# Performance work log

Hardware: AMD Instinct MI355X
Metric: run time of the kernel (lower is better)

Reference implementation:

```python
import jax, jax.numpy as jnp
import numpy as np

# CustomConvLayer with a 3x3-tap .kof file, global defaults:
#   operation: x * w, input_encode: x, kernel_encode: w
# => out[b,o,h,w] = sum_c sum_k x_pad[b,c,h+dh_k,w+dw_k] * weights[o,c,k]
# Tap offsets: integer stencil (dh,dw) in {0,1,2}^2 (k_elems=9), padding=1, stride=1.

PAD = 1
TAPS = [(dh, dw) for dh in range(3) for dw in range(3)]  # 9 taps


def setup_inputs() -> dict:
    key = jax.random.key(0)
    k1, k2 = jax.random.split(key)
    x = jax.random.normal(k1, (16, 64, 128, 128), dtype=jnp.float32)
    # learned per-tap weights: [out_channels, in_channels, k_elems]
    weights = jax.random.normal(k2, (128, 64, 9), dtype=jnp.float32) * 0.05
    return {"x": x, "weights": weights}


def reference(x, weights):
    B, C, H, Wd = x.shape
    xp = jnp.pad(x, ((0, 0), (0, 0), (PAD, PAD), (PAD, PAD)))
    # gather per-tap shifted views: [B, C, K, H, W]
    gathered = jnp.stack([xp[:, :, dh:dh + H, dw:dw + Wd] for dh, dw in TAPS], axis=2)
    # per-tap op x*w, then combine over in_channels and taps
    out = jnp.einsum('bckhw,ock->bohw', gathered, weights)
    return out
```

## Files before the change

### kernel.cpp

```cpp
#include <hip/hip_runtime.h>
#include <hip/hip_bf16.h>
#include <stdint.h>


typedef __bf16 bf16x8 __attribute__((ext_vector_type(8)));
typedef float  f32x4  __attribute__((ext_vector_type(4)));

#define GLD_TO_LDS16(g, l)                                                        \
  __builtin_amdgcn_global_load_lds((const __attribute__((address_space(1))) void*)(g), \
                                   (__attribute__((address_space(3))) void*)(l), 16, 0, 0)

__global__ __launch_bounds__(256) void xform_x(const float* __restrict__ x,
                                               __bf16* __restrict__ xpad) {
  __shared__ float tile[64][129];
  const int tid = threadIdx.x;
  const int b = blockIdx.x >> 7;
  const int h = blockIdx.x & 127;

  const bf16x8 z8 = {};
  __bf16* prow = xpad + (size_t)(b * 130 + h + 1) * 8320;
  if (tid < 8)        *(bf16x8*)(prow + tid * 8) = z8;
  else if (tid < 16)  *(bf16x8*)(prow + 8256 + (tid - 8) * 8) = z8;
  if (h == 0) {
    bf16x8* r0 = (bf16x8*)(xpad + (size_t)(b * 130) * 8320);
    for (int i = tid; i < 1040; i += 256) r0[i] = z8;
  } else if (h == 127) {
    bf16x8* r129 = (bf16x8*)(xpad + (size_t)(b * 130 + 129) * 8320);
    for (int i = tid; i < 1040; i += 256) r129[i] = z8;
  }

  const float* src = x + (((size_t)b * 64) * 128 + h) * 128;
  for (int i = tid; i < 2048; i += 256) {
    const int c = i >> 5, w4 = i & 31;
    f32x4 v = *(const f32x4*)(src + (size_t)c * 16384 + w4 * 4);
    tile[c][w4 * 4 + 0] = v[0];
    tile[c][w4 * 4 + 1] = v[1];
    tile[c][w4 * 4 + 2] = v[2];
    tile[c][w4 * 4 + 3] = v[3];
  }
  __syncthreads();
  __bf16* dst = xpad + ((size_t)(b * 130 + h + 1) * 130 + 1) * 64;
  for (int i = tid; i < 1024; i += 256) {
    const int w = i >> 3, cg = i & 7;
    bf16x8 o;
#pragma unroll
    for (int r = 0; r < 8; ++r) o[r] = (__bf16)tile[cg * 8 + r][w];
    *(bf16x8*)(dst + (size_t)w * 64 + cg * 8) = o;
  }
}

__global__ __launch_bounds__(256) void xform_w(const float* __restrict__ wgt,
                                               __bf16* __restrict__ BtF) {
  const int t = blockIdx.x * 256 + threadIdx.x;
  if (t >= 9216) return;
  const int s = t >> 9, rem = t & 511, quad = rem >> 7, n = rem & 127;
  bf16x8 o;
#pragma unroll
  for (int r = 0; r < 8; ++r) {
    const int k = s * 32 + quad * 8 + r;
    const int tap = k >> 6, c = k & 63;
    o[r] = (__bf16)wgt[(n * 64 + c) * 9 + tap];
  }
  *(bf16x8*)(BtF + (size_t)t * 8) = o;
}

__global__ __launch_bounds__(512, 4) void conv_mfma(const __bf16* __restrict__ xpad,
                                                    const __bf16* __restrict__ BtF,
                                                    float* __restrict__ out) {
  __shared__ alignas(16) __bf16 Aslab[4160 * 8];
  const int tid  = threadIdx.x;
  const int lane = tid & 63;
  const int wave = tid >> 6;
  const int quad = lane >> 4;
  const int l16  = lane & 15;
  const int rank = (blockIdx.x & 7) * 128 + (blockIdx.x >> 3);
  const int b  = rank >> 6;
  const int h0 = (rank & 63) << 1;
  const int wn = wave & 1;
  const int wm = wave >> 1;
  const int r  = wm >> 1;
  const int wq = (wm & 1) << 6;

  const __bf16* slab = xpad + (size_t)(b * 130 + h0) * 8320;
#define STAGE_BLK(BLK) do {                                               \
    const int l_   = ((BLK) << 6) + lane;                                 \
    const int v_   = l_ >> 3;                                             \
    const int cqs_ = (l_ & 7) ^ (v_ & 7);                                 \
    GLD_TO_LDS16(slab + v_ * 64 + cqs_ * 8, (char*)Aslab + ((BLK) << 10)); \
  } while (0)

#pragma unroll
  for (int k = 0; k < 4; ++k) STAGE_BLK(wave + (k << 3));
  STAGE_BLK(32);
  __builtin_amdgcn_sched_barrier(0);
  STAGE_BLK(33 + wave * 2);
  STAGE_BLK(34 + wave * 2);
  __builtin_amdgcn_sched_barrier(0);
  STAGE_BLK(49 + wave * 2);
  STAGE_BLK(50 + wave * 2);
  __builtin_amdgcn_sched_barrier(0);

  f32x4 acc[4][4] = {};

#define PHASE(DH)                                                              \
  _Pragma("unroll")                                                            \
  for (int dw = 0; dw < 3; ++dw) {                                             \
    _Pragma("unroll")                                                          \
    for (int half = 0; half < 2; ++half) {                                     \
      const int s_  = ((DH) * 3 + dw) * 2 + half;                              \
      const int cq_ = (half << 2) + quad;                                      \
      bf16x8 aF[4], bF[4];          \
      _Pragma("unroll")                                                        \
      for (int i = 0; i < 4; ++i) {                                            \
        const int v_    = ((DH) + r) * 130 + wq + (i << 4) + l16 + dw;         \
        const int slot_ = (v_ << 3) + (cq_ ^ (v_ & 7));                        \
        aF[i] = *(const bf16x8*)(Aslab + (size_t)slot_ * 8);                   \
        bF[i] = *(const bf16x8*)(BtF +                                         \
                 ((size_t)((s_ * 4 + quad) * 128 + (wn << 6) + (i << 4) + l16) << 3)); \
      }                                                                        \
      _Pragma("unroll")                                                        \
      for (int i = 0; i < 4; ++i)                                              \
        _Pragma("unroll")                                                      \
        for (int j = 0; j < 4; ++j)                                            \
          acc[i][j] = __builtin_amdgcn_mfma_f32_16x16x32_bf16(aF[i], bF[j],    \
                                                              acc[i][j], 0, 0, 0); \
    }                                                                          \
  }

  asm volatile("s_waitcnt vmcnt(4)" ::: "memory");
  __builtin_amdgcn_s_barrier();
  PHASE(0)
  asm volatile("s_waitcnt vmcnt(2)" ::: "memory");
  __builtin_amdgcn_s_barrier();
  PHASE(1)
  asm volatile("s_waitcnt vmcnt(0)" ::: "memory");
  __builtin_amdgcn_s_barrier();
  PHASE(2)

#pragma unroll
  for (int j = 0; j < 4; ++j) {
    const int n = (wn << 6) + (j << 4) + l16;
    float* orow = out + (((size_t)(b * 128 + n) * 128 + (h0 + r)) << 7);
#pragma unroll
    for (int i = 0; i < 4; ++i) {
      const int m0 = wq + (i << 4) + (quad << 2);
      *(f32x4*)(orow + m0) = acc[i][j];
    }
  }
}

__global__ void conv_naive(const float* __restrict__ x, const float* __restrict__ wgt,
                           float* __restrict__ out, int total) {
  int idx = blockIdx.x * 256 + threadIdx.x;
  if (idx >= total) return;
  const int w = idx & 127;
  const int h = (idx >> 7) & 127;
  const int o = (idx >> 14) & 127;
  const int b = idx >> 21;
  float s = 0.f;
  for (int c = 0; c < 64; ++c) {
    const float* xc = x + ((size_t)(b * 64 + c) * 128) * 128;
    const float* wc = wgt + (o * 64 + c) * 9;
    for (int dh = 0; dh < 3; ++dh) {
      const int hh = h + dh - 1;
      if (hh < 0 || hh >= 128) continue;
      for (int dw = 0; dw < 3; ++dw) {
        const int ww = w + dw - 1;
        if (ww < 0 || ww >= 128) continue;
        s += xc[hh * 128 + ww] * wc[dh * 3 + dw];
      }
    }
  }
  out[idx] = s;
}

extern "C" void kernel_launch(void* const* d_in, const int* in_sizes, int n_in,
                              void* d_out, int out_size, void* d_ws, size_t ws_size,
                              hipStream_t stream) {
  const float* x   = (const float*)d_in[0];
  const float* wgt = (const float*)d_in[1];
  float* out = (float*)d_out;

  const size_t BTF_BYTES  = 9216ull * 16;
  const size_t XPAD_BYTES = 16ull * 130 * 130 * 64 * sizeof(__bf16);

  if (ws_size < BTF_BYTES + XPAD_BYTES) {
    const int total = 16 * 128 * 128 * 128;
    conv_naive<<<(total + 255) / 256, 256, 0, stream>>>(x, wgt, out, total);
    return;
  }

  __bf16* BtF  = (__bf16*)d_ws;
  __bf16* xpad = (__bf16*)((char*)d_ws + BTF_BYTES);

  xform_w<<<36, 256, 0, stream>>>(wgt, BtF);
  xform_x<<<16 * 128, 256, 0, stream>>>(x, xpad);
  conv_mfma<<<1024, 512, 0, stream>>>(xpad, BtF, out);
}
```

Before: 221.0 us.

## Fuse input transpose/bf16 conversion into conv kernel, drop padded workspace

Removes the separate xform_x pass that wrote a padded NHWC bf16 copy of x, and instead has each conv block load three fp32 input rows directly, convert to bf16, and transpose through a double-buffered LDS tile into the swizzled A slab. Blocks now cover one output row with 256 threads instead of two rows with 512, and outputs use nontemporal stores. This removes the extra global round-trip and a kernel launch. In exchange each input row is read and converted by three blocks, and the staging loop has a barrier per step.

```diff
diff --git a/kernel.cpp b/kernel.cpp
--- a/kernel.cpp
+++ b/kernel.cpp
@@ -5,49 +5,6 @@
 
 typedef __bf16 bf16x8 __attribute__((ext_vector_type(8)));
 typedef float  f32x4  __attribute__((ext_vector_type(4)));
-
-#define GLD_TO_LDS16(g, l)                                                        \
-  __builtin_amdgcn_global_load_lds((const __attribute__((address_space(1))) void*)(g), \
-                                   (__attribute__((address_space(3))) void*)(l), 16, 0, 0)
-
-__global__ __launch_bounds__(256) void xform_x(const float* __restrict__ x,
-                                               __bf16* __restrict__ xpad) {
-  __shared__ float tile[64][129];
-  const int tid = threadIdx.x;
-  const int b = blockIdx.x >> 7;
-  const int h = blockIdx.x & 127;
-
-  const bf16x8 z8 = {};
-  __bf16* prow = xpad + (size_t)(b * 130 + h + 1) * 8320;
-  if (tid < 8)        *(bf16x8*)(prow + tid * 8) = z8;
-  else if (tid < 16)  *(bf16x8*)(prow + 8256 + (tid - 8) * 8) = z8;
-  if (h == 0) {
-    bf16x8* r0 = (bf16x8*)(xpad + (size_t)(b * 130) * 8320);
-    for (int i = tid; i < 1040; i += 256) r0[i] = z8;
-  } else if (h == 127) {
-    bf16x8* r129 = (bf16x8*)(xpad + (size_t)(b * 130 + 129) * 8320);
-    for (int i = tid; i < 1040; i += 256) r129[i] = z8;
-  }
-
-  const float* src = x + (((size_t)b * 64) * 128 + h) * 128;
-  for (int i = tid; i < 2048; i += 256) {
-    const int c = i >> 5, w4 = i & 31;
-    f32x4 v = *(const f32x4*)(src + (size_t)c * 16384 + w4 * 4);
-    tile[c][w4 * 4 + 0] = v[0];
-    tile[c][w4 * 4 + 1] = v[1];
-    tile[c][w4 * 4 + 2] = v[2];
-    tile[c][w4 * 4 + 3] = v[3];
-  }
-  __syncthreads();
-  __bf16* dst = xpad + ((size_t)(b * 130 + h + 1) * 130 + 1) * 64;
-  for (int i = tid; i < 1024; i += 256) {
-    const int w = i >> 3, cg = i & 7;
-    bf16x8 o;
-#pragma unroll
-    for (int r = 0; r < 8; ++r) o[r] = (__bf16)tile[cg * 8 + r][w];
-    *(bf16x8*)(dst + (size_t)w * 64 + cg * 8) = o;
-  }
-}
 
 __global__ __launch_bounds__(256) void xform_w(const float* __restrict__ wgt,
                                                __bf16* __restrict__ BtF) {
@@ -64,87 +21,108 @@
   *(bf16x8*)(BtF + (size_t)t * 8) = o;
 }
 
-__global__ __launch_bounds__(512, 4) void conv_mfma(const __bf16* __restrict__ xpad,
-                                                    const __bf16* __restrict__ BtF,
-                                                    float* __restrict__ out) {
-  __shared__ alignas(16) __bf16 Aslab[4160 * 8];
+__global__ __launch_bounds__(256) void conv_mfma(const float* __restrict__ x,
+                                                 const __bf16* __restrict__ BtF,
+                                                 float* __restrict__ out) {
+  __shared__ alignas(16) __bf16 Aslab[3120 * 8];
+  __shared__ alignas(16) __bf16 T[2][64][40];
   const int tid  = threadIdx.x;
   const int lane = tid & 63;
   const int wave = tid >> 6;
   const int quad = lane >> 4;
   const int l16  = lane & 15;
-  const int rank = (blockIdx.x & 7) * 128 + (blockIdx.x >> 3);
-  const int b  = rank >> 6;
-  const int h0 = (rank & 63) << 1;
+  const int rank = (blockIdx.x & 7) * 256 + (blockIdx.x >> 3);
+  const int b = rank >> 7;
+  const int h = rank & 127;
+  const int wm = wave >> 1;
   const int wn = wave & 1;
-  const int wm = wave >> 1;
-  const int r  = wm >> 1;
-  const int wq = (wm & 1) << 6;
 
-  const __bf16* slab = xpad + (size_t)(b * 130 + h0) * 8320;
-#define STAGE_BLK(BLK) do {                                               \
-    const int l_   = ((BLK) << 6) + lane;                                 \
-    const int v_   = l_ >> 3;                                             \
-    const int cqs_ = (l_ & 7) ^ (v_ & 7);                                 \
-    GLD_TO_LDS16(slab + v_ * 64 + cqs_ * 8, (char*)Aslab + ((BLK) << 10)); \
+  if (tid < 48) {
+    const int r3 = tid >> 4, wp = ((tid >> 3) & 1) * 129, cq = tid & 7;
+    const int v = r3 * 130 + wp;
+    const bf16x8 z = {};
+    *(bf16x8*)(Aslab + (size_t)(v * 8 + (cq ^ (v & 7))) * 8) = z;
+  }
+
+  const int cS   = tid >> 2;
+  const int wS   = (tid & 3) * 8;
+  const int wloc = tid & 31;
+  const int cqG  = tid >> 5;
+  const float* xc = x + ((size_t)b * 64 + cS) * 16384;
+
+  f32x4 g[3][2];
+
+#define XR_OF(u) (h - 1 + ((u) >> 2))
+#define ISSUE(u) do {                                                         \
+    const int xr_  = XR_OF(u);                                                \
+    const int xrc_ = xr_ < 0 ? 0 : (xr_ > 127 ? 127 : xr_);                   \
+    const float* p_ = xc + (size_t)xrc_ * 128 + ((u) & 3) * 32 + wS;          \
+    g[(u) % 3][0] = *(const f32x4*)p_;                                        \
+    g[(u) % 3][1] = *(const f32x4*)(p_ + 4);                                  \
   } while (0)
 
+  ISSUE(0);
+  ISSUE(1);
 #pragma unroll
-  for (int k = 0; k < 4; ++k) STAGE_BLK(wave + (k << 3));
-  STAGE_BLK(32);
-  __builtin_amdgcn_sched_barrier(0);
-  STAGE_BLK(33 + wave * 2);
-  STAGE_BLK(34 + wave * 2);
-  __builtin_amdgcn_sched_barrier(0);
-  STAGE_BLK(49 + wave * 2);
-  STAGE_BLK(50 + wave * 2);
+  for (int u = 0; u < 12; ++u) {
+    if (u < 10) ISSUE(u + 2);
+    {
+      const int xr_ = XR_OF(u);
+      f32x4 a0 = g[u % 3][0], a1 = g[u % 3][1];
+      if (xr_ < 0 || xr_ > 127) { a0 = (f32x4){}; a1 = (f32x4){}; }
+      bf16x8 pk;
+      pk[0] = (__bf16)a0[0]; pk[1] = (__bf16)a0[1];
+      pk[2] = (__bf16)a0[2]; pk[3] = (__bf16)a0[3];
+      pk[4] = (__bf16)a1[0]; pk[5] = (__bf16)a1[1];
+      pk[6] = (__bf16)a1[2]; pk[7] = (__bf16)a1[3];
+      *(bf16x8*)&T[u & 1][cS][wS] = pk;
+    }
+    asm volatile("s_waitcnt lgkmcnt(0)" ::: "memory");
+    __builtin_amdgcn_s_barrier();
+    __builtin_amdgcn_sched_barrier(0);
+    {
+      bf16x8 o;
+#pragma unroll
+      for (int j = 0; j < 8; ++j) o[j] = T[u & 1][cqG * 8 + j][wloc];
+      const int v = (u >> 2) * 130 + ((u & 3) << 5) + wloc + 1;
+      *(bf16x8*)(Aslab + (size_t)(v * 8 + (cqG ^ (v & 7))) * 8) = o;
+    }
+  }
+  asm volatile("s_waitcnt lgkmcnt(0)" ::: "memory");
+  __builtin_amdgcn_s_barrier();
   __builtin_amdgcn_sched_barrier(0);
 
   f32x4 acc[4][4] = {};
-
-#define PHASE(DH)                                                              \
-  _Pragma("unroll")                                                            \
-  for (int dw = 0; dw < 3; ++dw) {                                             \
-    _Pragma("unroll")                                                          \
-    for (int half = 0; half < 2; ++half) {                                     \
-      const int s_  = ((DH) * 3 + dw) * 2 + half;                              \
-      const int cq_ = (half << 2) + quad;                                      \
-      bf16x8 aF[4], bF[4];          \
-      _Pragma("unroll")                                                        \
-      for (int i = 0; i < 4; ++i) {                                            \
-        const int v_    = ((DH) + r) * 130 + wq + (i << 4) + l16 + dw;         \
-        const int slot_ = (v_ << 3) + (cq_ ^ (v_ & 7));                        \
-        aF[i] = *(const bf16x8*)(Aslab + (size_t)slot_ * 8);                   \
-        bF[i] = *(const bf16x8*)(BtF +                                         \
-                 ((size_t)((s_ * 4 + quad) * 128 + (wn << 6) + (i << 4) + l16) << 3)); \
-      }                                                                        \
-      _Pragma("unroll")                                                        \
-      for (int i = 0; i < 4; ++i)                                              \
-        _Pragma("unroll")                                                      \
-        for (int j = 0; j < 4; ++j)                                            \
-          acc[i][j] = __builtin_amdgcn_mfma_f32_16x16x32_bf16(aF[i], bF[j],    \
-                                                              acc[i][j], 0, 0, 0); \
-    }                                                                          \
+#pragma unroll
+  for (int s = 0; s < 18; ++s) {
+    const int tap = s >> 1;
+    const int dh = tap / 3, dw = tap % 3;
+    const int cq = ((s & 1) << 2) + quad;
+    bf16x8 aF[4], bF[4];
+#pragma unroll
+    for (int i = 0; i < 4; ++i) {
+      const int m = (wm << 6) + (i << 4) + l16;
+      const int v = dh * 130 + m + dw;
+      const int slot = (v << 3) + (cq ^ (v & 7));
+      aF[i] = *(const bf16x8*)(Aslab + (size_t)slot * 8);
+      const int n = (wn << 6) + (i << 4) + l16;
+      bF[i] = *(const bf16x8*)(BtF + ((size_t)((s * 4 + quad) * 128 + n) << 3));
+    }
+#pragma unroll
+    for (int i = 0; i < 4; ++i)
+#pragma unroll
+      for (int j = 0; j < 4; ++j)
+        acc[i][j] = __builtin_amdgcn_mfma_f32_16x16x32_bf16(aF[i], bF[j], acc[i][j], 0, 0, 0);
   }
-
-  asm volatile("s_waitcnt vmcnt(4)" ::: "memory");
-  __builtin_amdgcn_s_barrier();
-  PHASE(0)
-  asm volatile("s_waitcnt vmcnt(2)" ::: "memory");
-  __builtin_amdgcn_s_barrier();
-  PHASE(1)
-  asm volatile("s_waitcnt vmcnt(0)" ::: "memory");
-  __builtin_amdgcn_s_barrier();
-  PHASE(2)
 
 #pragma unroll
   for (int j = 0; j < 4; ++j) {
     const int n = (wn << 6) + (j << 4) + l16;
-    float* orow = out + (((size_t)(b * 128 + n) * 128 + (h0 + r)) << 7);
+    float* orow = out + (((size_t)(b * 128 + n) * 128 + h) << 7);
 #pragma unroll
     for (int i = 0; i < 4; ++i) {
-      const int m0 = wq + (i << 4) + (quad << 2);
-      *(f32x4*)(orow + m0) = acc[i][j];
+      const int m0 = (wm << 6) + (i << 4) + (quad << 2);
+      __builtin_nontemporal_store(acc[i][j], (f32x4*)(orow + m0));
     }
   }
 }
@@ -181,19 +159,16 @@
   const float* wgt = (const float*)d_in[1];
   float* out = (float*)d_out;
 
-  const size_t BTF_BYTES  = 9216ull * 16;
-  const size_t XPAD_BYTES = 16ull * 130 * 130 * 64 * sizeof(__bf16);
+  const size_t BTF_BYTES = 9216ull * 16;
 
-  if (ws_size < BTF_BYTES + XPAD_BYTES) {
+  if (ws_size < BTF_BYTES) {
     const int total = 16 * 128 * 128 * 128;
     conv_naive<<<(total + 255) / 256, 256, 0, stream>>>(x, wgt, out, total);
     return;
   }
 
-  __bf16* BtF  = (__bf16*)d_ws;
-  __bf16* xpad = (__bf16*)((char*)d_ws + BTF_BYTES);
+  __bf16* BtF = (__bf16*)d_ws;
 
   xform_w<<<36, 256, 0, stream>>>(wgt, BtF);
-  xform_x<<<16 * 128, 256, 0, stream>>>(x, xpad);
-  conv_mfma<<<1024, 512, 0, stream>>>(xpad, BtF, out);
+  conv_mfma<<<2048, 256, 0, stream>>>(x, BtF, out);
 }
```

Result: slower. 230.8 us (+4.4%).

## Fuse weight/input transforms and shrink conv blocks to one output row

Applied to the files above, without the earlier changes.

Merges the weight-transform kernel into the input-transform kernel, removing one launch. Retiles the MFMA conv from 512-thread blocks covering two output rows to 256-thread blocks covering one row, with a smaller 3-row LDS slab staged in 13 uniform units. This raises block count and LDS-limited occupancy, at the cost of more halo reloads per output row (3 rows staged per output row instead of 4 per 2) and more per-block overhead.

```diff
diff --git a/kernel.cpp b/kernel.cpp
--- a/kernel.cpp
+++ b/kernel.cpp
@@ -10,12 +10,29 @@
   __builtin_amdgcn_global_load_lds((const __attribute__((address_space(1))) void*)(g), \
                                    (__attribute__((address_space(3))) void*)(l), 16, 0, 0)
 
-__global__ __launch_bounds__(256) void xform_x(const float* __restrict__ x,
-                                               __bf16* __restrict__ xpad) {
+__global__ __launch_bounds__(256) void xform_xw(const float* __restrict__ x,
+                                                const float* __restrict__ wgt,
+                                                __bf16* __restrict__ xpad,
+                                                __bf16* __restrict__ BtF) {
   __shared__ float tile[64][129];
   const int tid = threadIdx.x;
   const int b = blockIdx.x >> 7;
   const int h = blockIdx.x & 127;
+
+  {
+    const int t = blockIdx.x * 256 + tid;
+    if (t < 9216) {
+      const int s = t >> 9, rem = t & 511, quad = rem >> 7, n = rem & 127;
+      bf16x8 o;
+#pragma unroll
+      for (int r = 0; r < 8; ++r) {
+        const int k = s * 32 + quad * 8 + r;
+        const int tap = k >> 6, c = k & 63;
+        o[r] = (__bf16)wgt[(n * 64 + c) * 9 + tap];
+      }
+      *(bf16x8*)(BtF + (size_t)t * 8) = o;
+    }
+  }
 
   const bf16x8 z8 = {};
   __bf16* prow = xpad + (size_t)(b * 130 + h + 1) * 8320;
@@ -49,55 +66,33 @@
   }
 }
 
-__global__ __launch_bounds__(256) void xform_w(const float* __restrict__ wgt,
-                                               __bf16* __restrict__ BtF) {
-  const int t = blockIdx.x * 256 + threadIdx.x;
-  if (t >= 9216) return;
-  const int s = t >> 9, rem = t & 511, quad = rem >> 7, n = rem & 127;
-  bf16x8 o;
-#pragma unroll
-  for (int r = 0; r < 8; ++r) {
-    const int k = s * 32 + quad * 8 + r;
-    const int tap = k >> 6, c = k & 63;
-    o[r] = (__bf16)wgt[(n * 64 + c) * 9 + tap];
-  }
-  *(bf16x8*)(BtF + (size_t)t * 8) = o;
-}
-
-__global__ __launch_bounds__(512, 4) void conv_mfma(const __bf16* __restrict__ xpad,
-                                                    const __bf16* __restrict__ BtF,
-                                                    float* __restrict__ out) {
-  __shared__ alignas(16) __bf16 Aslab[4160 * 8];
+__global__ __launch_bounds__(256) void conv_mfma(const __bf16* __restrict__ xpad,
+                                                 const __bf16* __restrict__ BtF,
+                                                 float* __restrict__ out) {
+  __shared__ alignas(16) __bf16 Aslab[3328 * 8];
   const int tid  = threadIdx.x;
   const int lane = tid & 63;
   const int wave = tid >> 6;
   const int quad = lane >> 4;
   const int l16  = lane & 15;
-  const int rank = (blockIdx.x & 7) * 128 + (blockIdx.x >> 3);
-  const int b  = rank >> 6;
-  const int h0 = (rank & 63) << 1;
+  const int rank = (blockIdx.x & 7) * 256 + (blockIdx.x >> 3);
+  const int b = rank >> 7;
+  const int h = rank & 127;
+  const int wm = wave >> 1;
   const int wn = wave & 1;
-  const int wm = wave >> 1;
-  const int r  = wm >> 1;
-  const int wq = (wm & 1) << 6;
 
-  const __bf16* slab = xpad + (size_t)(b * 130 + h0) * 8320;
-#define STAGE_BLK(BLK) do {                                               \
-    const int l_   = ((BLK) << 6) + lane;                                 \
+  const __bf16* slab = xpad + ((size_t)(b * 130 + h) * 130) * 64;
+#define STAGE_UNIT(U) do {                                                \
+    const int l_   = ((U) << 8) + tid;                                    \
     const int v_   = l_ >> 3;                                             \
+    const int vc_  = v_ > 389 ? 389 : v_;                                 \
     const int cqs_ = (l_ & 7) ^ (v_ & 7);                                 \
-    GLD_TO_LDS16(slab + v_ * 64 + cqs_ * 8, (char*)Aslab + ((BLK) << 10)); \
+    GLD_TO_LDS16(slab + vc_ * 64 + cqs_ * 8,                              \
+                 (char*)Aslab + ((((U) << 2) + wave) << 10));             \
   } while (0)
 
 #pragma unroll
-  for (int k = 0; k < 4; ++k) STAGE_BLK(wave + (k << 3));
-  STAGE_BLK(32);
-  __builtin_amdgcn_sched_barrier(0);
-  STAGE_BLK(33 + wave * 2);
-  STAGE_BLK(34 + wave * 2);
-  __builtin_amdgcn_sched_barrier(0);
-  STAGE_BLK(49 + wave * 2);
-  STAGE_BLK(50 + wave * 2);
+  for (int u = 0; u < 13; ++u) STAGE_UNIT(u);
   __builtin_amdgcn_sched_barrier(0);
 
   f32x4 acc[4][4] = {};
@@ -112,11 +107,12 @@
       bf16x8 aF[4], bF[4];          \
       _Pragma("unroll")                                                        \
       for (int i = 0; i < 4; ++i) {                                            \
-        const int v_    = ((DH) + r) * 130 + wq + (i << 4) + l16 + dw;         \
+        const int m_    = (wm << 6) + (i << 4) + l16;                          \
+        const int v_    = (DH) * 130 + m_ + dw;                                \
         const int slot_ = (v_ << 3) + (cq_ ^ (v_ & 7));                        \
         aF[i] = *(const bf16x8*)(Aslab + (size_t)slot_ * 8);                   \
-        bF[i] = *(const bf16x8*)(BtF +                                         \
-                 ((size_t)((s_ * 4 + quad) * 128 + (wn << 6) + (i << 4) + l16) << 3)); \
+        const int n_ = (wn << 6) + (i << 4) + l16;                             \
+        bF[i] = *(const bf16x8*)(BtF + ((size_t)((s_ * 4 + quad) * 128 + n_) << 3)); \
       }                                                                        \
       _Pragma("unroll")                                                        \
       for (int i = 0; i < 4; ++i)                                              \
@@ -127,23 +123,26 @@
     }                                                                          \
   }
 
+  asm volatile("s_waitcnt vmcnt(8)" ::: "memory");
+  __builtin_amdgcn_s_barrier();
+  __builtin_amdgcn_sched_barrier(0);
+  PHASE(0)
   asm volatile("s_waitcnt vmcnt(4)" ::: "memory");
   __builtin_amdgcn_s_barrier();
-  PHASE(0)
-  asm volatile("s_waitcnt vmcnt(2)" ::: "memory");
-  __builtin_amdgcn_s_barrier();
+  __builtin_amdgcn_sched_barrier(0);
   PHASE(1)
   asm volatile("s_waitcnt vmcnt(0)" ::: "memory");
   __builtin_amdgcn_s_barrier();
+  __builtin_amdgcn_sched_barrier(0);
   PHASE(2)
 
 #pragma unroll
   for (int j = 0; j < 4; ++j) {
     const int n = (wn << 6) + (j << 4) + l16;
-    float* orow = out + (((size_t)(b * 128 + n) * 128 + (h0 + r)) << 7);
+    float* orow = out + (((size_t)(b * 128 + n) * 128 + h) << 7);
 #pragma unroll
     for (int i = 0; i < 4; ++i) {
-      const int m0 = wq + (i << 4) + (quad << 2);
+      const int m0 = (wm << 6) + (i << 4) + (quad << 2);
       *(f32x4*)(orow + m0) = acc[i][j];
     }
   }
@@ -193,7 +192,6 @@
   __bf16* BtF  = (__bf16*)d_ws;
   __bf16* xpad = (__bf16*)((char*)d_ws + BTF_BYTES);
 
-  xform_w<<<36, 256, 0, stream>>>(wgt, BtF);
-  xform_x<<<16 * 128, 256, 0, stream>>>(x, xpad);
-  conv_mfma<<<1024, 512, 0, stream>>>(xpad, BtF, out);
+  xform_xw<<<16 * 128, 256, 0, stream>>>(x, wgt, xpad, BtF);
+  conv_mfma<<<16 * 128, 256, 0, stream>>>(xpad, BtF, out);
 }
```

New measurement: 215.6 us. 2.5% less time.
